# Optimization experiments

Hardware: AMD Instinct MI355X
Metric: run time of the kernel (lower is better)

Reference implementation:

```python
import jax, jax.numpy as jnp
import numpy as np

NUM_HEADS = 16
NEG_BIG = -1.0e9


def setup_inputs() -> dict:
    key = jax.random.key(0)
    k1, k2, k3 = jax.random.split(key, 3)
    B, S, D = 2, 2048, 1024
    x = jax.random.normal(k1, (B, S, D), dtype=jnp.float32)
    qkv_weights = jax.random.normal(k2, (D, 3 * D), dtype=jnp.float32) * (1.0 / np.sqrt(D))
    output_weights = jax.random.normal(k3, (D, D), dtype=jnp.float32) * (1.0 / np.sqrt(D))
    return {"x": x, "qkv_weights": qkv_weights, "output_weights": output_weights}


def reference(x, qkv_weights, output_weights):
    B, S, D = x.shape
    H = NUM_HEADS
    hd = D // H
    qkv = jnp.einsum('bsd,de->bse', x, qkv_weights)  # [B,S,3D]
    q, k, v = jnp.split(qkv, 3, axis=-1)
    # [B,H,S,hd]
    q = q.reshape(B, S, H, hd).transpose(0, 2, 1, 3)
    k = k.reshape(B, S, H, hd).transpose(0, 2, 1, 3)
    v = v.reshape(B, S, H, hd).transpose(0, 2, 1, 3)
    scores = jnp.einsum('bhqd,bhkd->bhqk', q, k)  # unscaled, matches original masked path
    # original bug: when masked, softmax is applied to UNSCALED scores with mask
    tril = jnp.tril(jnp.ones((S, S), dtype=scores.dtype))
    masked = scores * tril + NEG_BIG * (1.0 - tril)
    attn = jax.nn.softmax(masked, axis=-1)
    heads = jnp.einsum('bhqk,bhkd->bhqd', attn, v)  # [B,H,S,hd]
    merged = heads.transpose(0, 2, 1, 3).reshape(B, S, D)
    return jnp.einsum('bsd,de->bse', merged, output_weights)
```

## Files before the change

### kernel.cpp

```cpp
#include <hip/hip_runtime.h>
#include <stdint.h>

using u16 = unsigned short;
typedef __attribute__((ext_vector_type(8))) _Float16 half8;
typedef __attribute__((ext_vector_type(4))) float f32x4;
typedef __attribute__((ext_vector_type(4))) unsigned short u16x4;

#define S_LEN 2048
#define D_MODEL 1024
#define NHEAD 16
#define HDIM 64

__device__ __forceinline__ u16 f2h_bits(float f){
    _Float16 h = (_Float16)f;
    return __builtin_bit_cast(u16, h);
}
__device__ __forceinline__ float h2f_bits(u16 v){
    return (float)__builtin_bit_cast(_Float16, v);
}

typedef __attribute__((address_space(1))) void gvoid;
typedef __attribute__((address_space(3))) void lvoid;
__device__ __forceinline__ void gload_lds16(const u16* g, u16* l){
    __builtin_amdgcn_global_load_lds((gvoid*)(uintptr_t)g, (lvoid*)l, 16, 0, 0);
}

__global__ __launch_bounds__(256) void k_cvt(const float* __restrict__ x, u16* __restrict__ xh,
                                             const float* __restrict__ W0, u16* __restrict__ T0,
                                             const float* __restrict__ W1, u16* __restrict__ T1){
    __shared__ float tt[32][33];
    int blk = blockIdx.x;
    if (blk < 4096){
        int i = blk*256 + threadIdx.x;
        float4 v = reinterpret_cast<const float4*>(x)[i];
        u16x4 o;
        o.x = f2h_bits(v.x); o.y = f2h_bits(v.y); o.z = f2h_bits(v.z); o.w = f2h_bits(v.w);
        reinterpret_cast<u16x4*>(xh)[i] = o;
        return;
    }
    int wi = blk - 4096;
    int bx = wi & 127, ky = wi >> 7;
    const float* W; u16* WT; int N, n0;
    if (bx < 96){ W = W0; WT = T0; N = 3072; n0 = bx*32; }
    else        { W = W1; WT = T1; N = 1024; n0 = (bx-96)*32; }
    int k0 = ky*32;
    int tx = threadIdx.x & 31, ty = threadIdx.x >> 5;
    #pragma unroll
    for (int i=0;i<4;++i) tt[ty+8*i][tx] = W[(size_t)(k0+ty+8*i)*N + n0+tx];
    __syncthreads();
    #pragma unroll
    for (int i=0;i<4;++i) WT[(size_t)(n0+ty+8*i)*1024 + k0+tx] = f2h_bits(tt[tx][ty+8*i]);
}

template<int EPI, int BN>
__global__ __launch_bounds__(256) void k_gemm(const u16* __restrict__ A, const u16* __restrict__ BT,
                                              float* __restrict__ Cf, u16* __restrict__ Qh,
                                              u16* __restrict__ Kh, u16* __restrict__ Vt){
    constexpr int Kd = 1024;
    constexpr int NF = BN/32;
    __shared__ u16 As[2*128*32];
    __shared__ u16 Bs[2*128*32];
    int nwg = gridDim.x;
    int cpx = nwg >> 3;
    int wg  = ((int)blockIdx.x & 7)*cpx + ((int)blockIdx.x >> 3);
    int tm = wg & 31, tn = wg >> 5;
    int t = threadIdx.x;
    int w = t >> 6, lane = t & 63;
    int lr = lane & 15, lg = lane >> 4;
    int wm = (w>>1)*64, wn = (w&1)*(BN/2);
    int m0 = tm*128 + wm, n0 = tn*BN + wn;

    const u16* aG = A  + (size_t)(tm*128 + (t>>2))*Kd + (t&3)*8;
    const u16* bG = BT + (size_t)(tn*BN + (t>>2))*Kd + (t&3)*8;
    u16* aL = As + (t>>2)*32 + (t&3)*8;
    u16* bL = Bs + (t>>2)*32 + (t&3)*8;

    auto stage = [&](int buf, int kk){
        gload_lds16(aG + kk, aL + buf*4096);
        gload_lds16(aG + kk + (size_t)64*Kd, aL + buf*4096 + 64*32);
        gload_lds16(bG + kk, bL + buf*4096);
        if (BN == 128) gload_lds16(bG + kk + (size_t)64*Kd, bL + buf*4096 + 64*32);
    };

    f32x4 acc[4][NF];
    #pragma unroll
    for (int i=0;i<4;++i)
        #pragma unroll
        for (int j=0;j<NF;++j) acc[i][j] = (f32x4){0.f,0.f,0.f,0.f};

    stage(0, 0);
    __syncthreads();
    for (int kk=0; kk<Kd; kk+=32){
        int cur = (kk>>5) & 1;
        if (kk+32 < Kd) stage(cur^1, kk+32);

        half8 av[4], bv[NF];
        #pragma unroll
        for (int mf=0;mf<4;++mf) av[mf] = *reinterpret_cast<const half8*>(&As[cur*4096 + (wm+mf*16+lr)*32 + lg*8]);
        #pragma unroll
        for (int nf=0;nf<NF;++nf) bv[nf] = *reinterpret_cast<const half8*>(&Bs[cur*4096 + (wn+nf*16+lr)*32 + lg*8]);
        __builtin_amdgcn_s_setprio(1);
        #pragma unroll
        for (int mf=0;mf<4;++mf)
            #pragma unroll
            for (int nf=0;nf<NF;++nf)
                acc[mf][nf] = __builtin_amdgcn_mfma_f32_16x16x32_f16(av[mf], bv[nf], acc[mf][nf], 0,0,0);
        __builtin_amdgcn_s_setprio(0);
        __syncthreads();
    }

    if (EPI == 0){
        #pragma unroll
        for (int mf=0;mf<4;++mf)
            #pragma unroll
            for (int nf=0;nf<NF;++nf)
                #pragma unroll
                for (int j=0;j<4;++j)
                    Cf[(size_t)(m0+mf*16+lg*4+j)*D_MODEL + n0+nf*16+lr] = acc[mf][nf][j];
    } else {
        #pragma unroll
        for (int mf=0;mf<4;++mf){
            int r0 = m0 + mf*16 + lg*4;
            int b  = r0 >> 11, s = r0 & 2047;
            #pragma unroll
            for (int nf=0;nf<NF;++nf){
                int col = n0 + nf*16 + lr;
                int which = col >> 10;
                int d  = col & 1023;
                int h  = d >> 6, di = d & 63;
                int bh = b*NHEAD + h;
                if (which == 2){
                    u16x4 pv;
                    pv.x = f2h_bits(acc[mf][nf][0]);
                    pv.y = f2h_bits(acc[mf][nf][1]);
                    pv.z = f2h_bits(acc[mf][nf][2]);
                    pv.w = f2h_bits(acc[mf][nf][3]);
                    *reinterpret_cast<u16x4*>(Vt + ((size_t)bh*HDIM + di)*S_LEN + s) = pv;
                } else {
                    u16* dst = (which==0 ? Qh : Kh) + ((size_t)bh*S_LEN + s)*HDIM + di;
                    #pragma unroll
                    for (int j=0;j<4;++j) dst[(size_t)j*HDIM] = f2h_bits(acc[mf][nf][j]);
                }
            }
        }
    }
}

__global__ __launch_bounds__(256,3) void k_attn(const u16* __restrict__ Q, const u16* __restrict__ K,
                                                const u16* __restrict__ Vt, u16* __restrict__ Mg,
                                                u16* __restrict__ On, float* __restrict__ Ml,
                                                float* __restrict__ Ll){
    __shared__ u16 Kl[2*64*64];
    __shared__ u16 Vl[2*64*64];
    __shared__ u16 plds[4][32][72];
    int t = threadIdx.x;
    int w = t >> 6, lane = t & 63;
    int lr = lane & 15, lg = lane >> 4;
    int blk = blockIdx.x;
    int bh  = blk & 31;
    int p   = blk >> 5;
    int qb, ktLo, ktHi, part; bool split;
    if (p < 8)      { qb = p;    ktLo = 0;      ktHi = 2*p+2;   split = false; part = 0; }
    else if (p < 16){ qb = 23-p; ktLo = 0;      ktHi = qb+1;    split = true;  part = 0; }
    else            { qb = 31-p; ktLo = qb+1;   ktHi = 2*qb+2;  split = true;  part = 1; }
    int q0w = qb*128 + w*32;
    int b = bh >> 4, h = bh & 15;
    int pid = split ? ((bh<<3) + (qb-8))*2 + part : 0;
    const u16* Qp = Q  + (size_t)bh*S_LEN*HDIM;
    const u16* Kp = K  + (size_t)bh*S_LEN*HDIM;
    const u16* Vp = Vt + (size_t)bh*HDIM*S_LEN;

    int c0 = t, c1 = t + 256;
    int r0 = c0 >> 3, s0 = 8*((c0 & 7) ^ (r0 & 7));
    int r1 = c1 >> 3, s1 = 8*((c1 & 7) ^ (r1 & 7));
    const u16* Ks0 = Kp + (size_t)r0*HDIM + s0;
    const u16* Ks1 = Kp + (size_t)r1*HDIM + s1;
    const u16* Vs0 = Vp + (size_t)r0*S_LEN + s0;
    const u16* Vs1 = Vp + (size_t)r1*S_LEN + s1;
    u16* Kd0 = Kl + c0*8; u16* Kd1 = Kl + c1*8;
    u16* Vd0 = Vl + c0*8; u16* Vd1 = Vl + c1*8;

    auto stageKV = [&](int buf, int kt){
        int kbase = kt*64;
        gload_lds16(Ks0 + (size_t)kbase*HDIM, Kd0 + buf*4096);
        gload_lds16(Ks1 + (size_t)kbase*HDIM, Kd1 + buf*4096);
        gload_lds16(Vs0 + kbase, Vd0 + buf*4096);
        gload_lds16(Vs1 + kbase, Vd1 + buf*4096);
    };

    half8 qf[2][2];
    #pragma unroll
    for (int qi=0;qi<2;++qi)
        #pragma unroll
        for (int ks=0;ks<2;++ks){
            half8 v = *reinterpret_cast<const half8*>(Qp + (size_t)(q0w+qi*16+lr)*HDIM + ks*32 + lg*8);
            #pragma unroll
            for (int j=0;j<8;++j) v[j] = v[j] * (_Float16)1.44269504f;
            qf[qi][ks] = v;
        }

    f32x4 oacc[2][4];
    float mrow[2], lrow[2];
    #pragma unroll
    for (int mf=0;mf<2;++mf){
        #pragma unroll
        for (int nf=0;nf<4;++nf) oacc[mf][nf] = (f32x4){0.f,0.f,0.f,0.f};
        mrow[mf] = -1e30f; lrow[mf] = 0.f;
    }

    int lastkt = (q0w + 31) >> 6;
    int swz = (lr & 7)*8;
    int nT = ktHi - ktLo;

    stageKV(0, ktLo);
    __syncthreads();
    for (int i=0; i<nT; ++i){
        int kt = ktLo + i;
        int cur = i & 1;
        if (i+1 < nT) stageKV(cur^1, kt+1);

        if (kt <= lastkt){
            const u16* Kb = Kl + cur*4096;
            const u16* Vb = Vl + cur*4096;
            int kbase = kt*64;
            half8 kfr[4][2];
            #pragma unroll
            for (int kf=0;kf<4;++kf)
                #pragma unroll
                for (int ks=0;ks<2;++ks)
                    kfr[kf][ks] = *reinterpret_cast<const half8*>(Kb + (kf*16+lr)*64 + ((ks*32 + lg*8) ^ swz));
            f32x4 sc[4][2];
            #pragma unroll
            for (int kf=0;kf<4;++kf)
                #pragma unroll
                for (int qi=0;qi<2;++qi) sc[kf][qi] = (f32x4){0.f,0.f,0.f,0.f};
            __builtin_amdgcn_s_setprio(1);
            #pragma unroll
            for (int kf=0;kf<4;++kf)
                #pragma unroll
                for (int qi=0;qi<2;++qi)
                    #pragma unroll
                    for (int ks=0;ks<2;++ks)
                        sc[kf][qi] = __builtin_amdgcn_mfma_f32_16x16x32_f16(kfr[kf][ks], qf[qi][ks], sc[kf][qi], 0,0,0);
            __builtin_amdgcn_s_setprio(0);

            half8 vf[4][2];
            #pragma unroll
            for (int nf=0;nf<4;++nf)
                #pragma unroll
                for (int kh=0;kh<2;++kh)
                    vf[nf][kh] = *reinterpret_cast<const half8*>(Vb + (nf*16+lr)*64 + ((kh*32 + lg*8) ^ swz));

            if (kt == lastkt){
                #pragma unroll
                for (int kf=0;kf<4;++kf)
                    #pragma unroll
                    for (int qi=0;qi<2;++qi)
                        #pragma unroll
                        for (int j=0;j<4;++j)
                            if (kbase+kf*16+lg*4+j > q0w+qi*16+lr) sc[kf][qi][j] = -1e9f;
            }

            float pmax[2];
            #pragma unroll
            for (int qi=0;qi<2;++qi){
                float t0 = fmaxf(fmaxf(sc[0][qi][0], sc[0][qi][1]), fmaxf(sc[0][qi][2], sc[0][qi][3]));
                float t1 = fmaxf(fmaxf(sc[1][qi][0], sc[1][qi][1]), fmaxf(sc[1][qi][2], sc[1][qi][3]));
                float t2 = fmaxf(fmaxf(sc[2][qi][0], sc[2][qi][1]), fmaxf(sc[2][qi][2], sc[2][qi][3]));
                float t3 = fmaxf(fmaxf(sc[3][qi][0], sc[3][qi][1]), fmaxf(sc[3][qi][2], sc[3][qi][3]));
                float tm = fmaxf(fmaxf(t0,t1), fmaxf(t2,t3));
                tm = fmaxf(tm, __shfl_xor(tm,16));
                tm = fmaxf(tm, __shfl_xor(tm,32));
                pmax[qi] = tm;
            }
            bool need = (pmax[0] > mrow[0]+8.0f) || (pmax[1] > mrow[1]+8.0f);
            if (__any(need)){
                float aq[2];
                #pragma unroll
                for (int qi=0;qi<2;++qi){
                    float mnew = fmaxf(mrow[qi], pmax[qi]);
                    aq[qi] = __builtin_amdgcn_exp2f(mrow[qi] - mnew);
                    mrow[qi] = mnew;
                    lrow[qi] *= aq[qi];
                }
                float am[2][4];
                #pragma unroll
                for (int mf=0;mf<2;++mf)
                    #pragma unroll
                    for (int j=0;j<4;++j) am[mf][j] = __shfl(aq[mf], lg*4+j);
                #pragma unroll
                for (int mf=0;mf<2;++mf)
                    #pragma unroll
                    for (int nf=0;nf<4;++nf)
                        #pragma unroll
                        for (int j=0;j<4;++j) oacc[mf][nf][j] *= am[mf][j];
            }
            #pragma unroll
            for (int qi=0;qi<2;++qi){
                float m = mrow[qi];
                float rs = 0.f;
                #pragma unroll
                for (int kf=0;kf<4;++kf)
                    #pragma unroll
                    for (int j=0;j<4;++j){
                        float e = __builtin_amdgcn_exp2f(sc[kf][qi][j] - m);
                        sc[kf][qi][j] = e;
                        rs += e;
                    }
                rs += __shfl_xor(rs,16);
                rs += __shfl_xor(rs,32);
                lrow[qi] += rs;
            }
            #pragma unroll
            for (int kf=0;kf<4;++kf)
                #pragma unroll
                for (int qi=0;qi<2;++qi){
                    u16x4 pk;
                    pk.x = f2h_bits(sc[kf][qi][0]);
                    pk.y = f2h_bits(sc[kf][qi][1]);
                    pk.z = f2h_bits(sc[kf][qi][2]);
                    pk.w = f2h_bits(sc[kf][qi][3]);
                    *reinterpret_cast<u16x4*>(&plds[w][qi*16+lr][kf*16+lg*4]) = pk;
                }
            half8 pa[2][2];
            #pragma unroll
            for (int mf=0;mf<2;++mf)
                #pragma unroll
                for (int kh=0;kh<2;++kh)
                    pa[mf][kh] = *reinterpret_cast<const half8*>(&plds[w][mf*16+lr][kh*32 + lg*8]);
            __builtin_amdgcn_s_setprio(1);
            #pragma unroll
            for (int mf=0;mf<2;++mf)
                #pragma unroll
                for (int nf=0;nf<4;++nf)
                    #pragma unroll
                    for (int kh=0;kh<2;++kh)
                        oacc[mf][nf] = __builtin_amdgcn_mfma_f32_16x16x32_f16(pa[mf][kh], vf[nf][kh], oacc[mf][nf], 0,0,0);
            __builtin_amdgcn_s_setprio(0);
        }
        __syncthreads();
    }

    float linv[2][4];
    #pragma unroll
    for (int mf=0;mf<2;++mf)
        #pragma unroll
        for (int j=0;j<4;++j) linv[mf][j] = 1.0f/__shfl(lrow[mf], lg*4+j);
    if (!split){
        #pragma unroll
        for (int mf=0;mf<2;++mf)
            #pragma unroll
            for (int nf=0;nf<4;++nf)
                #pragma unroll
                for (int j=0;j<4;++j)
                    Mg[(size_t)(b*S_LEN + q0w + mf*16 + lg*4 + j)*D_MODEL + h*HDIM + nf*16 + lr]
                        = f2h_bits(oacc[mf][nf][j]*linv[mf][j]);
    } else {
        #pragma unroll
        for (int mf=0;mf<2;++mf)
            #pragma unroll
            for (int nf=0;nf<4;++nf)
                #pragma unroll
                for (int j=0;j<4;++j)
                    On[pid*8192 + (w*32 + mf*16 + lg*4 + j)*64 + nf*16 + lr]
                        = f2h_bits(oacc[mf][nf][j]*linv[mf][j]);
        if (lg == 0){
            #pragma unroll
            for (int qi=0;qi<2;++qi){
                Ml[pid*128 + w*32 + qi*16 + lr] = mrow[qi];
                Ll[pid*128 + w*32 + qi*16 + lr] = lrow[qi];
            }
        }
    }
}

__global__ __launch_bounds__(256) void k_comb(const u16* __restrict__ On, const float* __restrict__ Ml,
                                              const float* __restrict__ Ll, u16* __restrict__ Mg){
    int blk = blockIdx.x;
    int bh = blk & 31;
    int q8 = (blk >> 5) & 7;
    int rq = blk >> 8;
    int qb = 8 + q8;
    int b = bh >> 4, h = bh & 15;
    int t = threadIdx.x;
    int r  = rq*16 + (t >> 4);
    int cc = (t & 15) * 4;
    int pid0 = ((bh<<3) + q8)*2, pid1 = pid0 + 1;
    float m1 = Ml[pid0*128 + r], m2 = Ml[pid1*128 + r];
    float l1 = Ll[pid0*128 + r], l2 = Ll[pid1*128 + r];
    float M  = fmaxf(m1, m2);
    float w1 = l1*__builtin_amdgcn_exp2f(m1 - M);
    float w2 = l2*__builtin_amdgcn_exp2f(m2 - M);
    float inv = 1.0f/(w1 + w2);
    u16x4 o1 = *reinterpret_cast<const u16x4*>(On + (size_t)pid0*8192 + r*64 + cc);
    u16x4 o2 = *reinterpret_cast<const u16x4*>(On + (size_t)pid1*8192 + r*64 + cc);
    u16x4 o;
    #pragma unroll
    for (int j=0;j<4;++j)
        o[j] = f2h_bits((w1*h2f_bits(o1[j]) + w2*h2f_bits(o2[j]))*inv);
    *reinterpret_cast<u16x4*>(Mg + (size_t)(b*S_LEN + qb*128 + r)*D_MODEL + h*HDIM + cc) = o;
}

extern "C" void kernel_launch(void* const* d_in, const int* in_sizes, int n_in,
                              void* d_out, int out_size, void* d_ws, size_t ws_size,
                              hipStream_t stream) {
    const float* x    = (const float*)d_in[0];
    const float* wqkv = (const float*)d_in[1];
    const float* wout = (const float*)d_in[2];
    float* out = (float*)d_out;
    char* ws = (char*)d_ws;

    const size_t MB = 1u<<20;
    u16* xh     = (u16*)(ws + 0*MB);
    u16* wqkvT  = (u16*)(ws + 8*MB);
    u16* woutT  = (u16*)(ws + 14*MB);
    u16* Qh     = (u16*)(ws + 16*MB);
    u16* Kh     = (u16*)(ws + 24*MB);
    u16* Vt     = (u16*)(ws + 32*MB);
    u16* Mg     = (u16*)(ws + 40*MB);
    u16* On     = (u16*)(ws + 48*MB);
    float* Ml   = (float*)(ws + 56*MB);
    float* Ll   = (float*)(ws + 56*MB + 256*1024);

    k_cvt        <<<8192, 256, 0, stream>>>(x, xh, wqkv, wqkvT, wout, woutT);
    k_gemm<1,128><<<768, 256, 0, stream>>>(xh, wqkvT, nullptr, Qh, Kh, Vt);
    k_attn       <<<768, 256, 0, stream>>>(Qh, Kh, Vt, Mg, On, Ml, Ll);
    k_comb       <<<2048, 256, 0, stream>>>(On, Ml, Ll, Mg);
    k_gemm<0,64> <<<512, 256, 0, stream>>>(Mg, woutT, out, nullptr, nullptr, nullptr);
}
```

Measured before the change: 110.6 us.

## Fuse split-KV combine into attention kernel via atomic last-block-finishes flag

Removes the separate combine kernel launch. Each split attention block bumps a per-(head, query-block) counter after a threadfence, and whichever of the two partner blocks arrives second merges both partial outputs into the merged buffer. The counters are zeroed by one extra block appended to the conversion kernel. This saves one launch and its tail, at the cost of a fence and extra synchronisation, plus serialized merge work in the last-arriving blocks.

New measurement: 198.3 us. 1.79x slower.

```diff
diff --git a/kernel.cpp b/kernel.cpp
--- a/kernel.cpp
+++ b/kernel.cpp
@@ -27,9 +27,14 @@
 
 __global__ __launch_bounds__(256) void k_cvt(const float* __restrict__ x, u16* __restrict__ xh,
                                              const float* __restrict__ W0, u16* __restrict__ T0,
-                                             const float* __restrict__ W1, u16* __restrict__ T1){
+                                             const float* __restrict__ W1, u16* __restrict__ T1,
+                                             unsigned* __restrict__ flags){
     __shared__ float tt[32][33];
     int blk = blockIdx.x;
+    if (blk >= 8192){
+        if (threadIdx.x < 256) flags[threadIdx.x] = 0u;
+        return;
+    }
     if (blk < 4096){
         int i = blk*256 + threadIdx.x;
         float4 v = reinterpret_cast<const float4*>(x)[i];
@@ -149,23 +154,27 @@
 __global__ __launch_bounds__(256,3) void k_attn(const u16* __restrict__ Q, const u16* __restrict__ K,
                                                 const u16* __restrict__ Vt, u16* __restrict__ Mg,
                                                 u16* __restrict__ On, float* __restrict__ Ml,
-                                                float* __restrict__ Ll){
+                                                float* __restrict__ Ll, unsigned* __restrict__ flags){
     __shared__ u16 Kl[2*64*64];
     __shared__ u16 Vl[2*64*64];
     __shared__ u16 plds[4][32][72];
+    __shared__ unsigned oldv;
     int t = threadIdx.x;
     int w = t >> 6, lane = t & 63;
     int lr = lane & 15, lg = lane >> 4;
     int blk = blockIdx.x;
     int bh  = blk & 31;
     int p   = blk >> 5;
-    int qb, ktLo, ktHi, part; bool split;
-    if (p < 8)      { qb = p;    ktLo = 0;      ktHi = 2*p+2;   split = false; part = 0; }
+    int qb, ktLo, ktHi; bool split;
+    int part = 0;
+    if (p < 8)      { qb = p;    ktLo = 0;      ktHi = 2*p+2;   split = false; }
     else if (p < 16){ qb = 23-p; ktLo = 0;      ktHi = qb+1;    split = true;  part = 0; }
     else            { qb = 31-p; ktLo = qb+1;   ktHi = 2*qb+2;  split = true;  part = 1; }
+    (void)part;
     int q0w = qb*128 + w*32;
     int b = bh >> 4, h = bh & 15;
-    int pid = split ? ((bh<<3) + (qb-8))*2 + part : 0;
+    int fidx = (bh<<3) + (qb-8);
+    int pid = split ? fidx*2 + part : 0;
     const u16* Qp = Q  + (size_t)bh*S_LEN*HDIM;
     const u16* Kp = K  + (size_t)bh*S_LEN*HDIM;
     const u16* Vp = Vt + (size_t)bh*HDIM*S_LEN;
@@ -371,34 +380,34 @@
                 Ll[pid*128 + w*32 + qi*16 + lr] = lrow[qi];
             }
         }
-    }
-}
-
-__global__ __launch_bounds__(256) void k_comb(const u16* __restrict__ On, const float* __restrict__ Ml,
-                                              const float* __restrict__ Ll, u16* __restrict__ Mg){
-    int blk = blockIdx.x;
-    int bh = blk & 31;
-    int q8 = (blk >> 5) & 7;
-    int rq = blk >> 8;
-    int qb = 8 + q8;
-    int b = bh >> 4, h = bh & 15;
-    int t = threadIdx.x;
-    int r  = rq*16 + (t >> 4);
-    int cc = (t & 15) * 4;
-    int pid0 = ((bh<<3) + q8)*2, pid1 = pid0 + 1;
-    float m1 = Ml[pid0*128 + r], m2 = Ml[pid1*128 + r];
-    float l1 = Ll[pid0*128 + r], l2 = Ll[pid1*128 + r];
-    float M  = fmaxf(m1, m2);
-    float w1 = l1*__builtin_amdgcn_exp2f(m1 - M);
-    float w2 = l2*__builtin_amdgcn_exp2f(m2 - M);
-    float inv = 1.0f/(w1 + w2);
-    u16x4 o1 = *reinterpret_cast<const u16x4*>(On + (size_t)pid0*8192 + r*64 + cc);
-    u16x4 o2 = *reinterpret_cast<const u16x4*>(On + (size_t)pid1*8192 + r*64 + cc);
-    u16x4 o;
-    #pragma unroll
-    for (int j=0;j<4;++j)
-        o[j] = f2h_bits((w1*h2f_bits(o1[j]) + w2*h2f_bits(o2[j]))*inv);
-    *reinterpret_cast<u16x4*>(Mg + (size_t)(b*S_LEN + qb*128 + r)*D_MODEL + h*HDIM + cc) = o;
+        __threadfence();
+        __syncthreads();
+        if (t == 0) oldv = atomicAdd(&flags[fidx], 1u);
+        __syncthreads();
+        if (oldv == 1u){
+            __threadfence();
+            int pid0 = fidx*2, pid1 = pid0 + 1;
+            #pragma unroll
+            for (int it=0; it<8; ++it){
+                int idx = it*256 + t;
+                int r  = idx >> 4;
+                int cc = (idx & 15)*4;
+                float m1 = Ml[pid0*128 + r], m2 = Ml[pid1*128 + r];
+                float l1 = Ll[pid0*128 + r], l2 = Ll[pid1*128 + r];
+                float M  = fmaxf(m1, m2);
+                float w1 = l1*__builtin_amdgcn_exp2f(m1 - M);
+                float w2 = l2*__builtin_amdgcn_exp2f(m2 - M);
+                float inv = 1.0f/(w1 + w2);
+                u16x4 o1 = *reinterpret_cast<const u16x4*>(On + (size_t)pid0*8192 + r*64 + cc);
+                u16x4 o2 = *reinterpret_cast<const u16x4*>(On + (size_t)pid1*8192 + r*64 + cc);
+                u16x4 o;
+                #pragma unroll
+                for (int j=0;j<4;++j)
+                    o[j] = f2h_bits((w1*h2f_bits(o1[j]) + w2*h2f_bits(o2[j]))*inv);
+                *reinterpret_cast<u16x4*>(Mg + (size_t)(b*S_LEN + qb*128 + r)*D_MODEL + h*HDIM + cc) = o;
+            }
+        }
+    }
 }
 
 extern "C" void kernel_launch(void* const* d_in, const int* in_sizes, int n_in,
@@ -411,20 +420,20 @@
     char* ws = (char*)d_ws;
 
     const size_t MB = 1u<<20;
-    u16* xh     = (u16*)(ws + 0*MB);
-    u16* wqkvT  = (u16*)(ws + 8*MB);
-    u16* woutT  = (u16*)(ws + 14*MB);
-    u16* Qh     = (u16*)(ws + 16*MB);
-    u16* Kh     = (u16*)(ws + 24*MB);
-    u16* Vt     = (u16*)(ws + 32*MB);
-    u16* Mg     = (u16*)(ws + 40*MB);
-    u16* On     = (u16*)(ws + 48*MB);
-    float* Ml   = (float*)(ws + 56*MB);
-    float* Ll   = (float*)(ws + 56*MB + 256*1024);
-
-    k_cvt        <<<8192, 256, 0, stream>>>(x, xh, wqkv, wqkvT, wout, woutT);
+    u16* xh      = (u16*)(ws + 0*MB);
+    u16* wqkvT   = (u16*)(ws + 8*MB);
+    u16* woutT   = (u16*)(ws + 14*MB);
+    u16* Qh      = (u16*)(ws + 16*MB);
+    u16* Kh      = (u16*)(ws + 24*MB);
+    u16* Vt      = (u16*)(ws + 32*MB);
+    u16* Mg      = (u16*)(ws + 40*MB);
+    u16* On      = (u16*)(ws + 48*MB);
+    float* Ml    = (float*)(ws + 56*MB);
+    float* Ll    = (float*)(ws + 56*MB + 256*1024);
+    unsigned* fl = (unsigned*)(ws + 56*MB + 512*1024);
+
+    k_cvt        <<<8193, 256, 0, stream>>>(x, xh, wqkv, wqkvT, wout, woutT, fl);
     k_gemm<1,128><<<768, 256, 0, stream>>>(xh, wqkvT, nullptr, Qh, Kh, Vt);
-    k_attn       <<<768, 256, 0, stream>>>(Qh, Kh, Vt, Mg, On, Ml, Ll);
-    k_comb       <<<2048, 256, 0, stream>>>(On, Ml, Ll, Mg);
+    k_attn       <<<768, 256, 0, stream>>>(Qh, Kh, Vt, Mg, On, Ml, Ll, fl);
     k_gemm<0,64> <<<512, 256, 0, stream>>>(Mg, woutT, out, nullptr, nullptr, nullptr);
 }
```
